# Kernel optimization log

Measured on AMD Instinct MI355X. Metric: run time of the kernel, lower is better.

The kernel has to match this reference:

```python
import jax, jax.numpy as jnp
import numpy as np

D_MODEL = 1024
NHEAD = 16
HEAD_DIM = D_MODEL // NHEAD
MAX_LEN = 4096
ROPE_BASE = 500.0


def _rope_tables(L, dim):
    inv_freq = 1.0 / (ROPE_BASE ** (jnp.arange(0, dim, 2, dtype=jnp.float32) / dim))
    t = jnp.arange(L, dtype=jnp.float32)
    freqs = jnp.einsum('i,j->ij', t, inv_freq)  # [L, dim/2]
    emb = jnp.concatenate([freqs, freqs], axis=-1)  # [L, dim]
    return jnp.cos(emb), jnp.sin(emb)


def _rotate_half(x):
    x1, x2 = jnp.split(x, 2, axis=-1)
    return jnp.concatenate([-x2, x1], axis=-1)


def _apply_rope(x, cos, sin):
    return x * cos + _rotate_half(x) * sin


def setup_inputs() -> dict:
    key = jax.random.key(0)
    ks = jax.random.split(key, 6)
    B, L = 4, 2048
    bound_qkv = 1.0 / np.sqrt(D_MODEL)
    x = jax.random.normal(ks[0], (B, L, D_MODEL), dtype=jnp.float32)
    key_padding_mask = jnp.zeros((B, L), dtype=bool)
    W_qkv = jax.random.uniform(ks[1], (3 * D_MODEL, D_MODEL), jnp.float32, -bound_qkv, bound_qkv)
    b_qkv = jax.random.uniform(ks[2], (3 * D_MODEL,), jnp.float32, -bound_qkv, bound_qkv)
    W_out = jax.random.uniform(ks[3], (D_MODEL, D_MODEL), jnp.float32, -bound_qkv, bound_qkv)
    b_out = jax.random.uniform(ks[4], (D_MODEL,), jnp.float32, -bound_qkv, bound_qkv)
    return {"x": x, "key_padding_mask": key_padding_mask,
            "W_qkv": W_qkv, "b_qkv": b_qkv, "W_out": W_out, "b_out": b_out}


def reference(x, key_padding_mask, W_qkv, b_qkv, W_out, b_out):
    B, L, D = x.shape
    H, hd = NHEAD, HEAD_DIM
    qkv = x @ W_qkv.T + b_qkv  # [B, L, 3D]
    q, k, v = jnp.split(qkv, 3, axis=-1)
    # [B, H, L, hd]
    q = q.reshape(B, L, H, hd).transpose(0, 2, 1, 3)
    k = k.reshape(B, L, H, hd).transpose(0, 2, 1, 3)
    v = v.reshape(B, L, H, hd).transpose(0, 2, 1, 3)
    cos, sin = _rope_tables(L, hd)  # [L, hd]
    q = _apply_rope(q, cos, sin)
    k = _apply_rope(k, cos, sin)
    scores = jnp.einsum('bhqd,bhkd->bhqk', q, k) / jnp.sqrt(jnp.float32(hd))
    mask = key_padding_mask[:, None, None, :]  # [B,1,1,L]
    scores = jnp.where(mask, -jnp.inf, scores)
    attn = jax.nn.softmax(scores, axis=-1)
    out = jnp.einsum('bhqk,bhkd->bhqd', attn, v)
    out = out.transpose(0, 2, 1, 3).reshape(B, L, D)
    return out @ W_out.T + b_out
```

## Files before the change

kernel.cpp:

```cpp
#include <hip/hip_runtime.h>
#include <stdint.h>

typedef __attribute__((ext_vector_type(8))) __bf16 bf16x8;
typedef __attribute__((ext_vector_type(4))) short short4v;
typedef __attribute__((ext_vector_type(4))) float f32x4;

#if __has_builtin(__builtin_amdgcn_exp2f)
#define EXP2(x) __builtin_amdgcn_exp2f(x)
#else
#define EXP2(x) exp2f(x)
#endif

__device__ __forceinline__ short f2bf(float f) {
  union { float f; uint32_t u; } v; v.f = f;
  uint32_t r = (v.u + 0x7fffu + ((v.u >> 16) & 1u)) >> 16;
  return (short)(uint16_t)r;
}

__device__ __forceinline__ uint32_t pk2bf(float a, float b) {
  union { __bf16 h; uint16_t u; } x, y;
  x.h = (__bf16)a; y.h = (__bf16)b;
  return (uint32_t)x.u | ((uint32_t)y.u << 16);
}

__device__ __forceinline__ void gl2lds16(const void* g, const void* lds) {
  __builtin_amdgcn_global_load_lds(
      (const __attribute__((address_space(1))) void*)(uintptr_t)g,
      (__attribute__((address_space(3))) void*)(uint32_t)(uintptr_t)lds,
      16, 0, 0);
}

__device__ __forceinline__ bf16x8 frag8(const short* p) {
  return *(const bf16x8*)(const void*)p;
}

__global__ void convert3_k(const float* __restrict__ s0, short* __restrict__ d0, int n0,
                           const float* __restrict__ s1, short* __restrict__ d1, int n1,
                           const float* __restrict__ s2, short* __restrict__ d2, int n2) {
  int i = blockIdx.x * blockDim.x + threadIdx.x;
  int t0 = n0 >> 2, t1 = t0 + (n1 >> 2), t2 = t1 + (n2 >> 2);
  const float* s; short* d; int off;
  if (i < t0) { s = s0; d = d0; off = i; }
  else if (i < t1) { s = s1; d = d1; off = i - t0; }
  else if (i < t2) { s = s2; d = d2; off = i - t1; }
  else return;
  float4 v = ((const float4*)s)[off];
  short4v o;
  o.x = f2bf(v.x); o.y = f2bf(v.y); o.z = f2bf(v.z); o.w = f2bf(v.w);
  *(short4v*)(d + off * 4) = o;
}

__global__ void rope_tab_k(float* __restrict__ cosT, float* __restrict__ sinT,
                           const unsigned char* __restrict__ mask, float* __restrict__ maskf) {
  int i = blockIdx.x * blockDim.x + threadIdx.x;
  int pos = i >> 5, j = i & 31;
  float invf = exp2f(-(float)j * (8.965784284662087f / 32.0f));
  float ang = (float)pos * invf;
  float s, c;
  sincosf(ang, &s, &c);
  cosT[i] = c; sinT[i] = s;
  if (i < 8192) maskf[i] = mask[i] ? -1e30f : 0.0f;
}

template <int EPI>
__global__ __launch_bounds__(256, 3)
void gemm_bt_k(const short* __restrict__ A, const short* __restrict__ Bm,
               const float* __restrict__ bias, int N, int K,
               float* __restrict__ Cout,
               const float* __restrict__ cosT, const float* __restrict__ sinT,
               short* __restrict__ Qb, short* __restrict__ Kb, short* __restrict__ Vt) {
  __shared__ short As[2][128 * 32];
  __shared__ short Bs[2][128 * 32];
  const int tid = threadIdx.x;
  const int lane = tid & 63;
  const int w = tid >> 6;
  const int g = lane >> 4, l15 = lane & 15;
  const int wm = (w >> 1) * 64, wn = (w & 1) * 64;
  const int bm = blockIdx.x, bn = blockIdx.y;

  const int rseg = lane >> 2;
  const int cofs = ((lane & 3) ^ ((lane >> 3) & 3)) * 8;
  const int sA0 = w, sA1 = w + 4;
  const int arow0 = (bm * 128 + sA0 * 16 + rseg) * K;
  const int arow1 = (bm * 128 + sA1 * 16 + rseg) * K;
  const int brow0 = (bn * 128 + sA0 * 16 + rseg) * K;
  const int brow1 = (bn * 128 + sA1 * 16 + rseg) * K;

  const int rsw = (l15 >> 1) & 3;

  f32x4 acc[4][4];
#pragma unroll
  for (int i = 0; i < 4; i++)
#pragma unroll
    for (int j = 0; j < 4; j++) acc[i][j] = f32x4{0.f, 0.f, 0.f, 0.f};

  gl2lds16(A + arow0 + cofs, &As[0][sA0 * 512]);
  gl2lds16(A + arow1 + cofs, &As[0][sA1 * 512]);
  gl2lds16(Bm + brow0 + cofs, &Bs[0][sA0 * 512]);
  gl2lds16(Bm + brow1 + cofs, &Bs[0][sA1 * 512]);

  int cur = 0;
  for (int k0 = 0; k0 < K; k0 += 32, cur ^= 1) {
    __syncthreads();
    int nxt = cur ^ 1;
    int k1 = k0 + 32;
    if (k1 < K) {
      gl2lds16(A + arow0 + k1 + cofs, &As[nxt][sA0 * 512]);
      gl2lds16(A + arow1 + k1 + cofs, &As[nxt][sA1 * 512]);
      gl2lds16(Bm + brow0 + k1 + cofs, &Bs[nxt][sA0 * 512]);
      gl2lds16(Bm + brow1 + k1 + cofs, &Bs[nxt][sA1 * 512]);
    }
    bf16x8 af[4], bf[4];
#pragma unroll
    for (int im = 0; im < 4; im++) af[im] = frag8(&As[cur][(wm + im * 16 + l15) * 32 + (g ^ rsw) * 8]);
#pragma unroll
    for (int jn = 0; jn < 4; jn++) bf[jn] = frag8(&Bs[cur][(wn + jn * 16 + l15) * 32 + (g ^ rsw) * 8]);
#pragma unroll
    for (int im = 0; im < 4; im++)
#pragma unroll
      for (int jn = 0; jn < 4; jn++)
        acc[im][jn] = __builtin_amdgcn_mfma_f32_16x16x32_bf16(af[im], bf[jn], acc[im][jn], 0, 0, 0);
  }

  const int row0 = bm * 128 + wm + g * 4;
  const int col0 = bn * 128 + wn;

  if (EPI == 0) {
#pragma unroll
    for (int jn = 0; jn < 4; jn++) {
      float bb = bias[col0 + jn * 16 + l15];
#pragma unroll
      for (int im = 0; im < 4; im++)
#pragma unroll
        for (int r = 0; r < 4; r++) {
          int row = row0 + im * 16 + r;
          Cout[row * N + col0 + jn * 16 + l15] = acc[im][jn][r] + bb;
        }
    }
  } else {
#pragma unroll
    for (int jn = 0; jn < 4; jn++) {
      float bb = bias[col0 + jn * 16 + l15];
#pragma unroll
      for (int im = 0; im < 4; im++)
#pragma unroll
        for (int r = 0; r < 4; r++) acc[im][jn][r] += bb;
    }
    const int sector = col0 >> 10;
    const int h = (col0 & 1023) >> 6;
    if (sector == 2) {
#pragma unroll
      for (int jn = 0; jn < 4; jn++) {
        int d = jn * 16 + l15;
#pragma unroll
        for (int im = 0; im < 4; im++) {
          int row = row0 + im * 16;
          int b = row >> 11, pos = row & 2047;
          union { uint32_t u[2]; short4v s4; } pw;
          pw.u[0] = pk2bf(acc[im][jn][0], acc[im][jn][1]);
          pw.u[1] = pk2bf(acc[im][jn][2], acc[im][jn][3]);
          *(short4v*)&Vt[((b * 16 + h) * 64 + d) * 2048 + pos] = pw.s4;
        }
      }
    } else {
      short* dst = (sector == 0) ? Qb : Kb;
      const float scl = (sector == 0) ? 0.18033688011112042f : 1.0f;
#pragma unroll
      for (int jn = 0; jn < 4; jn++) {
        int d = jn * 16 + l15;
        int j = d & 31;
#pragma unroll
        for (int im = 0; im < 4; im++)
#pragma unroll
          for (int r = 0; r < 4; r++) {
            int row = row0 + im * 16 + r;
            int b = row >> 11, pos = row & 2047;
            float c = cosT[pos * 32 + j];
            float s = sinT[pos * 32 + j];
            float xv = acc[im][jn][r];
            float xp = acc[im][jn ^ 2][r];
            float rot = (jn < 2) ? -xp : xp;
            dst[((b * 16 + h) * 2048 + pos) * 64 + d] = f2bf((xv * c + rot * s) * scl);
          }
      }
    }
  }
}

__global__ __launch_bounds__(128, 4)
void attn_k(const short* __restrict__ Qb, const short* __restrict__ Kb,
            const short* __restrict__ Vt, const float* __restrict__ maskf,
            short* __restrict__ attn) {
  __shared__ short Ks[2][32 * 64];
  __shared__ short Vs[2][64 * 32];
  __shared__ short Ps[2][32 * 32];
  const int tid = threadIdx.x, lane = tid & 63, w = tid >> 6;
  const int g = lane >> 4, l15 = lane & 15;
  const int swk = l15 & 7;
  const int fv = (l15 ^ (l15 >> 2)) & 3;
  const int qt = blockIdx.x, bh = blockIdx.y;
  const int b = bh >> 4, h = bh & 15;

  bf16x8 aq[2][2];
#pragma unroll
  for (int qi = 0; qi < 2; qi++)
#pragma unroll
    for (int kc = 0; kc < 2; kc++) {
      int q = qt * 64 + w * 32 + qi * 16 + l15;
      aq[qi][kc] = *(const bf16x8*)(const void*)(Qb + (bh * 2048 + q) * 64 + kc * 32 + g * 8);
    }
  bf16x8 aone;
#pragma unroll
  for (int i = 0; i < 8; i++) aone[i] = (__bf16)1.0f;

  f32x4 o[4][2];
#pragma unroll
  for (int jd = 0; jd < 4; jd++)
#pragma unroll
    for (int qi = 0; qi < 2; qi++) o[jd][qi] = f32x4{0.f, 0.f, 0.f, 0.f};
  f32x4 lacc[2] = {f32x4{0.f, 0.f, 0.f, 0.f}, f32x4{0.f, 0.f, 0.f, 0.f}};

  const float* mfp = maskf + b * 2048;

  const int kr8 = lane >> 3;
  const int kcst = (lane & 7) ^ kr8;
  const int vrs = lane >> 2;
  const int vcs = (lane & 3) ^ ((vrs ^ (vrs >> 2)) & 3);

  if (w == 0) {
#pragma unroll
    for (int s = 0; s < 4; s++)
      gl2lds16(Kb + (bh * 2048 + s * 8 + kr8) * 64 + kcst * 8, &Ks[0][s * 512]);
  } else {
#pragma unroll
    for (int s = 0; s < 4; s++)
      gl2lds16(Vt + (bh * 64 + s * 16 + vrs) * 2048 + vcs * 8, &Vs[0][s * 512]);
  }

  int cur = 0;
  for (int kt = 0; kt < 64; kt++, cur ^= 1) {
    const int kbase = kt * 32;
    __syncthreads();
    int nxt = cur ^ 1;
    if (kt + 1 < 64) {
      const int nb = kbase + 32;
      if (w == 0) {
#pragma unroll
        for (int s = 0; s < 4; s++)
          gl2lds16(Kb + (bh * 2048 + nb + s * 8 + kr8) * 64 + kcst * 8, &Ks[nxt][s * 512]);
      } else {
#pragma unroll
        for (int s = 0; s < 4; s++)
          gl2lds16(Vt + (bh * 64 + s * 16 + vrs) * 2048 + nb + vcs * 8, &Vs[nxt][s * 512]);
      }
    }

    f32x4 sv[2][2];
#pragma unroll
    for (int kvt = 0; kvt < 2; kvt++) {
      f32x4 mf = *(const f32x4*)(mfp + kbase + kvt * 16 + g * 4);
      sv[kvt][0] = mf; sv[kvt][1] = mf;
    }
#pragma unroll
    for (int kvt = 0; kvt < 2; kvt++)
#pragma unroll
      for (int kc = 0; kc < 2; kc++) {
        bf16x8 ak = frag8(&Ks[cur][(kvt * 16 + l15) * 64 + ((kc * 4 + g) ^ swk) * 8]);
        sv[kvt][0] = __builtin_amdgcn_mfma_f32_16x16x32_bf16(ak, aq[0][kc], sv[kvt][0], 0, 0, 0);
        sv[kvt][1] = __builtin_amdgcn_mfma_f32_16x16x32_bf16(ak, aq[1][kc], sv[kvt][1], 0, 0, 0);
      }

#pragma unroll
    for (int qi = 0; qi < 2; qi++)
#pragma unroll
      for (int kvt = 0; kvt < 2; kvt++) {
        union { uint32_t u[2]; short4v s4; } pw;
        pw.u[0] = pk2bf(EXP2(sv[kvt][qi][0]), EXP2(sv[kvt][qi][1]));
        pw.u[1] = pk2bf(EXP2(sv[kvt][qi][2]), EXP2(sv[kvt][qi][3]));
        *(short4v*)&Ps[w][(qi * 16 + l15) * 32 + (((kvt * 2 + (g >> 1)) ^ fv) * 8) + (g & 1) * 4] = pw.s4;
      }

    {
      bf16x8 av[4];
#pragma unroll
      for (int jd = 0; jd < 4; jd++)
        av[jd] = frag8(&Vs[cur][(jd * 16 + l15) * 32 + (g ^ fv) * 8]);
#pragma unroll
      for (int qi = 0; qi < 2; qi++) {
        bf16x8 bp = frag8(&Ps[w][(qi * 16 + l15) * 32 + (g ^ fv) * 8]);
#pragma unroll
        for (int jd = 0; jd < 4; jd++)
          o[jd][qi] = __builtin_amdgcn_mfma_f32_16x16x32_bf16(av[jd], bp, o[jd][qi], 0, 0, 0);
        lacc[qi] = __builtin_amdgcn_mfma_f32_16x16x32_bf16(aone, bp, lacc[qi], 0, 0, 0);
      }
    }
  }

#pragma unroll
  for (int qi = 0; qi < 2; qi++) {
    float inv = 1.0f / lacc[qi][0];
    int q = qt * 64 + w * 32 + qi * 16 + l15;
#pragma unroll
    for (int jd = 0; jd < 4; jd++) {
      union { uint32_t u[2]; short4v s4; } pw;
      pw.u[0] = pk2bf(o[jd][qi][0] * inv, o[jd][qi][1] * inv);
      pw.u[1] = pk2bf(o[jd][qi][2] * inv, o[jd][qi][3] * inv);
      *(short4v*)&attn[(b * 2048 + q) * 1024 + h * 64 + jd * 16 + g * 4] = pw.s4;
    }
  }
}

extern "C" void kernel_launch(void* const* d_in, const int* in_sizes, int n_in,
                              void* d_out, int out_size, void* d_ws, size_t ws_size,
                              hipStream_t stream) {
  const float* x = (const float*)d_in[0];
  const unsigned char* mask = (const unsigned char*)d_in[1];
  const float* W_qkv = (const float*)d_in[2];
  const float* b_qkv = (const float*)d_in[3];
  const float* W_out = (const float*)d_in[4];
  const float* b_out = (const float*)d_in[5];
  float* out = (float*)d_out;

  char* ws = (char*)d_ws;
  short* xb    = (short*)(ws + 0);
  short* wqkvb = (short*)(ws + 16777216);
  short* woutb = (short*)(ws + 23068672);
  float* cosT  = (float*)(ws + 25165824);
  float* sinT  = (float*)(ws + 25427968);
  short* Qb    = (short*)(ws + 25690112);
  short* Kb    = (short*)(ws + 42467328);
  short* Vtb   = (short*)(ws + 59244544);
  short* attnb = (short*)(ws + 76021760);
  float* maskf = (float*)(ws + 92798976);

  convert3_k<<<12288, 256, 0, stream>>>(x, xb, 8388608, W_qkv, wqkvb, 3145728, W_out, woutb, 1048576);
  rope_tab_k<<<256, 256, 0, stream>>>(cosT, sinT, mask, maskf);
  gemm_bt_k<1><<<dim3(64, 24), 256, 0, stream>>>(xb, wqkvb, b_qkv, 3072, 1024,
                                                 nullptr, cosT, sinT, Qb, Kb, Vtb);
  attn_k<<<dim3(32, 64), 128, 0, stream>>>(Qb, Kb, Vtb, maskf, attnb);
  gemm_bt_k<0><<<dim3(64, 8), 256, 0, stream>>>(attnb, woutb, b_out, 1024, 1024,
                                                out, nullptr, nullptr, nullptr, nullptr, nullptr);
}
```

Baseline: 297.2 us.

## Widen attention blocks to four waves with triple-buffered KV and LDS mask

The attention kernel now runs 256 threads per block, with each block covering 128 queries, so each K/V tile loaded into LDS is shared by four waves instead of two. K/V staging moves from double to triple buffering with explicit vmcnt waits and raw barriers, so loads are issued two tiles ahead. The mask row is staged once into LDS, and MFMA sections are wrapped in s_setprio. A 1D grid with a block-index swizzle groups the query tiles of each head for L2 locality. The cost is more LDS per block, which may lower occupancy, and the waitcnt accounting depends on the exact number of outstanding loads.

```diff
diff --git a/kernel.cpp b/kernel.cpp
--- a/kernel.cpp
+++ b/kernel.cpp
@@ -187,18 +187,20 @@
   }
 }
 
-__global__ __launch_bounds__(128, 4)
+__global__ __launch_bounds__(256, 4)
 void attn_k(const short* __restrict__ Qb, const short* __restrict__ Kb,
             const short* __restrict__ Vt, const float* __restrict__ maskf,
             short* __restrict__ attn) {
-  __shared__ short Ks[2][32 * 64];
-  __shared__ short Vs[2][64 * 32];
-  __shared__ short Ps[2][32 * 32];
+  __shared__ short Ks[3][32 * 64];
+  __shared__ short Vs[3][64 * 32];
+  __shared__ short Ps[4][32 * 32];
+  __shared__ float Ms[2048];
   const int tid = threadIdx.x, lane = tid & 63, w = tid >> 6;
   const int g = lane >> 4, l15 = lane & 15;
   const int swk = l15 & 7;
   const int fv = (l15 ^ (l15 >> 2)) & 3;
-  const int qt = blockIdx.x, bh = blockIdx.y;
+  const int swz = (blockIdx.x & 7) * 128 + (blockIdx.x >> 3);
+  const int qt = swz & 15, bh = swz >> 4;
   const int b = bh >> 4, h = bh & 15;
 
   bf16x8 aq[2][2];
@@ -206,7 +208,7 @@
   for (int qi = 0; qi < 2; qi++)
 #pragma unroll
     for (int kc = 0; kc < 2; kc++) {
-      int q = qt * 64 + w * 32 + qi * 16 + l15;
+      int q = qt * 128 + w * 32 + qi * 16 + l15;
       aq[qi][kc] = *(const bf16x8*)(const void*)(Qb + (bh * 2048 + q) * 64 + kc * 32 + g * 8);
     }
   bf16x8 aone;
@@ -227,40 +229,63 @@
   const int vrs = lane >> 2;
   const int vcs = (lane & 3) ^ ((vrs ^ (vrs >> 2)) & 3);
 
-  if (w == 0) {
-#pragma unroll
-    for (int s = 0; s < 4; s++)
-      gl2lds16(Kb + (bh * 2048 + s * 8 + kr8) * 64 + kcst * 8, &Ks[0][s * 512]);
+#pragma unroll
+  for (int i = 0; i < 2; i++) {
+    int s = w * 2 + i;
+    gl2lds16(mfp + s * 256 + lane * 4, &Ms[s * 256]);
+  }
+  if (w < 2) {
+#pragma unroll
+    for (int t = 0; t < 2; t++)
+#pragma unroll
+      for (int i = 0; i < 2; i++) {
+        int s = (w & 1) * 2 + i;
+        gl2lds16(Kb + (bh * 2048 + t * 32 + s * 8 + kr8) * 64 + kcst * 8, &Ks[t][s * 512]);
+      }
   } else {
 #pragma unroll
-    for (int s = 0; s < 4; s++)
-      gl2lds16(Vt + (bh * 64 + s * 16 + vrs) * 2048 + vcs * 8, &Vs[0][s * 512]);
-  }
-
-  int cur = 0;
-  for (int kt = 0; kt < 64; kt++, cur ^= 1) {
+    for (int t = 0; t < 2; t++)
+#pragma unroll
+      for (int i = 0; i < 2; i++) {
+        int s = (w & 1) * 2 + i;
+        gl2lds16(Vt + (bh * 64 + s * 16 + vrs) * 2048 + t * 32 + vcs * 8, &Vs[t][s * 512]);
+      }
+  }
+
+  int cur = 0, pre = 2;
+  for (int kt = 0; kt < 64; kt++) {
+    if (kt < 62) {
+      asm volatile("s_waitcnt vmcnt(2)" ::: "memory");
+    } else {
+      asm volatile("s_waitcnt vmcnt(0)" ::: "memory");
+    }
+    __builtin_amdgcn_s_barrier();
+
+    if (kt < 62) {
+      const int nb = (kt + 2) * 32;
+      if (w < 2) {
+#pragma unroll
+        for (int i = 0; i < 2; i++) {
+          int s = (w & 1) * 2 + i;
+          gl2lds16(Kb + (bh * 2048 + nb + s * 8 + kr8) * 64 + kcst * 8, &Ks[pre][s * 512]);
+        }
+      } else {
+#pragma unroll
+        for (int i = 0; i < 2; i++) {
+          int s = (w & 1) * 2 + i;
+          gl2lds16(Vt + (bh * 64 + s * 16 + vrs) * 2048 + nb + vcs * 8, &Vs[pre][s * 512]);
+        }
+      }
+    }
+
     const int kbase = kt * 32;
-    __syncthreads();
-    int nxt = cur ^ 1;
-    if (kt + 1 < 64) {
-      const int nb = kbase + 32;
-      if (w == 0) {
-#pragma unroll
-        for (int s = 0; s < 4; s++)
-          gl2lds16(Kb + (bh * 2048 + nb + s * 8 + kr8) * 64 + kcst * 8, &Ks[nxt][s * 512]);
-      } else {
-#pragma unroll
-        for (int s = 0; s < 4; s++)
-          gl2lds16(Vt + (bh * 64 + s * 16 + vrs) * 2048 + nb + vcs * 8, &Vs[nxt][s * 512]);
-      }
-    }
-
     f32x4 sv[2][2];
 #pragma unroll
     for (int kvt = 0; kvt < 2; kvt++) {
-      f32x4 mf = *(const f32x4*)(mfp + kbase + kvt * 16 + g * 4);
+      f32x4 mf = *(const f32x4*)(const void*)&Ms[kbase + kvt * 16 + g * 4];
       sv[kvt][0] = mf; sv[kvt][1] = mf;
     }
+    __builtin_amdgcn_s_setprio(1);
 #pragma unroll
     for (int kvt = 0; kvt < 2; kvt++)
 #pragma unroll
@@ -269,6 +294,7 @@
         sv[kvt][0] = __builtin_amdgcn_mfma_f32_16x16x32_bf16(ak, aq[0][kc], sv[kvt][0], 0, 0, 0);
         sv[kvt][1] = __builtin_amdgcn_mfma_f32_16x16x32_bf16(ak, aq[1][kc], sv[kvt][1], 0, 0, 0);
       }
+    __builtin_amdgcn_s_setprio(0);
 
 #pragma unroll
     for (int qi = 0; qi < 2; qi++)
@@ -285,6 +311,7 @@
 #pragma unroll
       for (int jd = 0; jd < 4; jd++)
         av[jd] = frag8(&Vs[cur][(jd * 16 + l15) * 32 + (g ^ fv) * 8]);
+      __builtin_amdgcn_s_setprio(1);
 #pragma unroll
       for (int qi = 0; qi < 2; qi++) {
         bf16x8 bp = frag8(&Ps[w][(qi * 16 + l15) * 32 + (g ^ fv) * 8]);
@@ -293,13 +320,17 @@
           o[jd][qi] = __builtin_amdgcn_mfma_f32_16x16x32_bf16(av[jd], bp, o[jd][qi], 0, 0, 0);
         lacc[qi] = __builtin_amdgcn_mfma_f32_16x16x32_bf16(aone, bp, lacc[qi], 0, 0, 0);
       }
-    }
+      __builtin_amdgcn_s_setprio(0);
+    }
+
+    cur = (cur == 2) ? 0 : cur + 1;
+    pre = (pre == 2) ? 0 : pre + 1;
   }
 
 #pragma unroll
   for (int qi = 0; qi < 2; qi++) {
     float inv = 1.0f / lacc[qi][0];
-    int q = qt * 64 + w * 32 + qi * 16 + l15;
+    int q = qt * 128 + w * 32 + qi * 16 + l15;
 #pragma unroll
     for (int jd = 0; jd < 4; jd++) {
       union { uint32_t u[2]; short4v s4; } pw;
@@ -337,7 +368,7 @@
   rope_tab_k<<<256, 256, 0, stream>>>(cosT, sinT, mask, maskf);
   gemm_bt_k<1><<<dim3(64, 24), 256, 0, stream>>>(xb, wqkvb, b_qkv, 3072, 1024,
                                                  nullptr, cosT, sinT, Qb, Kb, Vtb);
-  attn_k<<<dim3(32, 64), 128, 0, stream>>>(Qb, Kb, Vtb, maskf, attnb);
+  attn_k<<<dim3(1024), 256, 0, stream>>>(Qb, Kb, Vtb, maskf, attnb);
   gemm_bt_k<0><<<dim3(64, 8), 256, 0, stream>>>(attnb, woutb, b_out, 1024, 1024,
                                                 out, nullptr, nullptr, nullptr, nullptr, nullptr);
 }
```

After: 287.2 us. 1.03x faster.
